# Performance work log

Hardware: AMD Instinct MI355X
Metric: run time of the kernel (lower is better)

## Reference

```python
import jax, jax.numpy as jnp
import numpy as np

B, H, W = 1, 64, 64  # N = B*H*W = 4096


def setup_inputs() -> dict:
    key = jax.random.key(0)
    pred_logits = jax.random.normal(key, (B, 1, H, W), dtype=jnp.float32)
    return {"pred_logits": pred_logits}


def _spectral_relaxation(feats):
    # feats: (N, 2) rows [max_conf, residual_dispersion]
    # L2-normalize rows (torch F.normalize: clamp norm at 1e-12)
    nrm = jnp.maximum(jnp.linalg.norm(feats, axis=1, keepdims=True), 1e-12)
    fn = feats / nrm
    A = fn @ fn.T                      # (N, N) rank<=2 gram affinity
    d = A.sum(axis=1)                  # degree vector
    dis = 1.0 / (jnp.sqrt(d) + 1e-10)  # D^{-1/2} diagonal
    # L_norm = D^{-1/2} (diag(d) - A) D^{-1/2}
    Ln = jnp.diag(d * dis * dis) - (dis[:, None] * A) * dis[None, :]
    w, V = jnp.linalg.eigh(Ln)
    fied = V[:, 1]                     # Fiedler vector (2nd smallest eigenvalue)
    # deterministic sign canonicalization (eigh sign is arbitrary)
    idx = jnp.argmax(jnp.abs(fied))
    fied = fied * jnp.where(fied[idx] >= 0, 1.0, -1.0)
    return (fied - fied.min()) / (fied.max() - fied.min() + 1e-10)


def reference(pred_logits):
    b, _, h, w = pred_logits.shape
    p = jax.nn.sigmoid(pred_logits)
    max_conf = jnp.maximum(p, 1.0 - p)               # (B,1,H,W)
    v = (1.0 - max_conf) / (max_conf + 1e-10)        # residual dispersion
    feats = jnp.concatenate([max_conf, v], axis=1)   # (B,2,H,W)
    feats_flat = feats.transpose(0, 2, 3, 1).reshape(-1, 2)  # (N,2)
    scores = _spectral_relaxation(feats_flat)        # (N,)
    reliability_mask = scores.reshape(b, h, w, 1).transpose(0, 3, 1, 2)
    return reliability_mask
```

## Files before the change

kernel.cpp:

```cpp
#include <hip/hip_runtime.h>
#include <math.h>


constexpr int N  = 4096;
constexpr int NT = 1024;
constexpr int PT = N / NT;
constexpr int NW = NT / 64;

__device__ __forceinline__ void block_reduce_sum(const double* vals, int m,
                                                 double* scr, double* outv) {
    const int lane = threadIdx.x & 63;
    const int wave = threadIdx.x >> 6;
    for (int j = 0; j < m; ++j) {
        double v = vals[j];
        #pragma unroll
        for (int off = 32; off > 0; off >>= 1) v += __shfl_down(v, off, 64);
        if (lane == 0) scr[j * NW + wave] = v;
    }
    __syncthreads();
    if (wave == 0) {
        for (int j = 0; j < m; ++j) {
            double v = (lane < NW) ? scr[j * NW + lane] : 0.0;
            #pragma unroll
            for (int off = 8; off > 0; off >>= 1) v += __shfl_down(v, off, 64);
            if (lane == 0) outv[j] = v;
        }
    }
    __syncthreads();
}

__global__ __launch_bounds__(NT) void spectral_kernel(const float* __restrict__ logits,
                                                      float* __restrict__ out) {
    __shared__ double s_scr[NW * 3];
    __shared__ double s_bc[4];
    __shared__ unsigned long long s_key[NW];
    __shared__ float s_mm[NW * 2];
    __shared__ float s_sign;

    const int tid  = threadIdx.x;
    const int lane = tid & 63;
    const int wave = tid >> 6;

    float c[PT], s[PT], dis[PT];

    double acc[3];
    acc[0] = 0.0; acc[1] = 0.0;
    #pragma unroll
    for (int k = 0; k < PT; ++k) {
        const int i = tid + k * NT;
        float x  = logits[i];
        float p  = 1.0f / (1.0f + expf(-x));
        float mc = fmaxf(p, 1.0f - p);
        float v  = (1.0f - mc) / (mc + 1e-10f);
        float nr = fmaxf(sqrtf(mc * mc + v * v), 1e-12f);
        c[k] = mc / nr;
        s[k] = v / nr;
        acc[0] += (double)c[k];
        acc[1] += (double)s[k];
    }
    block_reduce_sum(acc, 2, s_scr, s_bc);
    const double Sc = s_bc[0];
    const double Ss = s_bc[1];

    acc[0] = 0.0; acc[1] = 0.0; acc[2] = 0.0;
    #pragma unroll
    for (int k = 0; k < PT; ++k) {
        double d  = (double)c[k] * Sc + (double)s[k] * Ss;
        double di = 1.0 / (sqrt(d) + 1e-10);
        dis[k] = (float)di;
        double gc = di * (double)c[k];
        double gs = di * (double)s[k];
        acc[0] += gc * gc;
        acc[1] += gc * gs;
        acc[2] += gs * gs;
    }
    block_reduce_sum(acc, 3, s_scr, s_bc);
    const double C11 = s_bc[0], C12 = s_bc[1], C22 = s_bc[2];

    double tr   = C11 + C22;
    double df   = C11 - C22;
    double disc = sqrt(df * df + 4.0 * C12 * C12);
    double lmin = 0.5 * (tr - disc);
    double ux1 = C12,        uy1 = lmin - C11;
    double ux2 = lmin - C22, uy2 = C12;
    double n1 = ux1 * ux1 + uy1 * uy1;
    double n2 = ux2 * ux2 + uy2 * uy2;
    double ux, uy, nn;
    if (n1 >= n2) { ux = ux1; uy = uy1; nn = n1; }
    else          { ux = ux2; uy = uy2; nn = n2; }
    double inv = 1.0 / sqrt(nn > 1e-300 ? nn : 1e-300);
    ux *= inv; uy *= inv;
    double sfac = 1.0 / sqrt(lmin > 1e-300 ? lmin : 1e-300);

    float fl[PT];
    float vmin = 3.402823466e38f, vmax = -3.402823466e38f;
    unsigned long long key = 0ULL;
    #pragma unroll
    for (int k = 0; k < PT; ++k) {
        const unsigned i = (unsigned)(tid + k * NT);
        double fv = (double)dis[k] * ((double)c[k] * ux + (double)s[k] * uy) * sfac;
        float f = (float)fv;
        fl[k] = f;
        vmin = fminf(vmin, f);
        vmax = fmaxf(vmax, f);
        unsigned af = __float_as_uint(fabsf(f));
        unsigned long long kk =
            ((unsigned long long)af << 32) | (unsigned long long)(0xFFFFFFFFu - i);
        key = (kk > key) ? kk : key;
    }
    #pragma unroll
    for (int off = 32; off > 0; off >>= 1) {
        vmin = fminf(vmin, __shfl_down(vmin, off, 64));
        vmax = fmaxf(vmax, __shfl_down(vmax, off, 64));
        unsigned long long ok = __shfl_down(key, off, 64);
        key = (ok > key) ? ok : key;
    }
    if (lane == 0) { s_mm[wave] = vmin; s_mm[NW + wave] = vmax; s_key[wave] = key; }
    __syncthreads();
    if (wave == 0) {
        vmin = (lane < NW) ? s_mm[lane]      :  3.402823466e38f;
        vmax = (lane < NW) ? s_mm[NW + lane] : -3.402823466e38f;
        key  = (lane < NW) ? s_key[lane]     : 0ULL;
        #pragma unroll
        for (int off = 8; off > 0; off >>= 1) {
            vmin = fminf(vmin, __shfl_down(vmin, off, 64));
            vmax = fmaxf(vmax, __shfl_down(vmax, off, 64));
            unsigned long long ok = __shfl_down(key, off, 64);
            key = (ok > key) ? ok : key;
        }
        if (lane == 0) { s_mm[0] = vmin; s_mm[1] = vmax; s_key[0] = key; }
    }
    __syncthreads();
    vmin = s_mm[0]; vmax = s_mm[1]; key = s_key[0];
    const unsigned widx = 0xFFFFFFFFu - (unsigned)(key & 0xFFFFFFFFULL);

    #pragma unroll
    for (int k = 0; k < PT; ++k) {
        const unsigned i = (unsigned)(tid + k * NT);
        if (i == widx) s_sign = (fl[k] >= 0.0f) ? 1.0f : -1.0f;
    }
    __syncthreads();
    const float sgn  = s_sign;
    const float gmin = (sgn > 0.0f) ? vmin : -vmax;
    const float gmax = (sgn > 0.0f) ? vmax : -vmin;
    const float invr = 1.0f / (gmax - gmin + 1e-10f);

    #pragma unroll
    for (int k = 0; k < PT; ++k) {
        const int i = tid + k * NT;
        out[i] = (sgn * fl[k] - gmin) * invr;
    }
}

extern "C" void kernel_launch(void* const* d_in, const int* in_sizes, int n_in,
                              void* d_out, int out_size, void* d_ws, size_t ws_size,
                              hipStream_t stream) {
    const float* logits = (const float*)d_in[0];
    float* out = (float*)d_out;
    spectral_kernel<<<dim3(1), dim3(NT), 0, stream>>>(logits, out);
}
```

Before: 60.35 us.

## Use float reductions, float4 I/O, fast exp, and pack sign into argmax key

Replaces the double-precision per-element math and block reductions with float arithmetic, keeping only the tiny 2x2 eigen solve in double. Loads and stores switch to float4 so each thread handles four contiguous elements. expf becomes __expf. The sign of the largest-magnitude entry is packed into the argmax key, which removes a shared write and one barrier. Together these aim to cut FP64 throughput cost and synchronization in this single-block kernel, at the risk of small precision differences against the reference.

```diff
diff --git a/kernel.cpp b/kernel.cpp
--- a/kernel.cpp
+++ b/kernel.cpp
@@ -7,12 +7,12 @@
 constexpr int PT = N / NT;
 constexpr int NW = NT / 64;
 
-__device__ __forceinline__ void block_reduce_sum(const double* vals, int m,
-                                                 double* scr, double* outv) {
+__device__ __forceinline__ void block_reduce_sum_f(const float* vals, int m,
+                                                   float* scr, float* outv) {
     const int lane = threadIdx.x & 63;
     const int wave = threadIdx.x >> 6;
     for (int j = 0; j < m; ++j) {
-        double v = vals[j];
+        float v = vals[j];
         #pragma unroll
         for (int off = 32; off > 0; off >>= 1) v += __shfl_down(v, off, 64);
         if (lane == 0) scr[j * NW + wave] = v;
@@ -20,7 +20,7 @@
     __syncthreads();
     if (wave == 0) {
         for (int j = 0; j < m; ++j) {
-            double v = (lane < NW) ? scr[j * NW + lane] : 0.0;
+            float v = (lane < NW) ? scr[j * NW + lane] : 0.0f;
             #pragma unroll
             for (int off = 8; off > 0; off >>= 1) v += __shfl_down(v, off, 64);
             if (lane == 0) outv[j] = v;
@@ -29,13 +29,12 @@
     __syncthreads();
 }
 
-__global__ __launch_bounds__(NT) void spectral_kernel(const float* __restrict__ logits,
-                                                      float* __restrict__ out) {
-    __shared__ double s_scr[NW * 3];
-    __shared__ double s_bc[4];
+__global__ __launch_bounds__(NT) void spectral_kernel(const float4* __restrict__ logits4,
+                                                      float4* __restrict__ out4) {
+    __shared__ float s_scr[NW * 3];
+    __shared__ float s_bc[4];
     __shared__ unsigned long long s_key[NW];
     __shared__ float s_mm[NW * 2];
-    __shared__ float s_sign;
 
     const int tid  = threadIdx.x;
     const int lane = tid & 63;
@@ -43,40 +42,41 @@
 
     float c[PT], s[PT], dis[PT];
 
-    double acc[3];
-    acc[0] = 0.0; acc[1] = 0.0;
+    const float4 x4 = logits4[tid];
+    const float xs[PT] = {x4.x, x4.y, x4.z, x4.w};
+    float acc[3];
+    acc[0] = 0.0f; acc[1] = 0.0f;
     #pragma unroll
     for (int k = 0; k < PT; ++k) {
-        const int i = tid + k * NT;
-        float x  = logits[i];
-        float p  = 1.0f / (1.0f + expf(-x));
+        float x  = xs[k];
+        float p  = 1.0f / (1.0f + __expf(-x));
         float mc = fmaxf(p, 1.0f - p);
         float v  = (1.0f - mc) / (mc + 1e-10f);
         float nr = fmaxf(sqrtf(mc * mc + v * v), 1e-12f);
         c[k] = mc / nr;
         s[k] = v / nr;
-        acc[0] += (double)c[k];
-        acc[1] += (double)s[k];
+        acc[0] += c[k];
+        acc[1] += s[k];
     }
-    block_reduce_sum(acc, 2, s_scr, s_bc);
-    const double Sc = s_bc[0];
-    const double Ss = s_bc[1];
+    block_reduce_sum_f(acc, 2, s_scr, s_bc);
+    const float Sc = s_bc[0];
+    const float Ss = s_bc[1];
 
-    acc[0] = 0.0; acc[1] = 0.0; acc[2] = 0.0;
+    acc[0] = 0.0f; acc[1] = 0.0f; acc[2] = 0.0f;
     #pragma unroll
     for (int k = 0; k < PT; ++k) {
-        double d  = (double)c[k] * Sc + (double)s[k] * Ss;
-        double di = 1.0 / (sqrt(d) + 1e-10);
-        dis[k] = (float)di;
-        double gc = di * (double)c[k];
-        double gs = di * (double)s[k];
+        float d  = c[k] * Sc + s[k] * Ss;
+        float di = 1.0f / (sqrtf(d) + 1e-10f);
+        dis[k] = di;
+        float gc = di * c[k];
+        float gs = di * s[k];
         acc[0] += gc * gc;
         acc[1] += gc * gs;
         acc[2] += gs * gs;
     }
-    block_reduce_sum(acc, 3, s_scr, s_bc);
-    const double C11 = s_bc[0], C12 = s_bc[1], C22 = s_bc[2];
+    block_reduce_sum_f(acc, 3, s_scr, s_bc);
 
+    const double C11 = (double)s_bc[0], C12 = (double)s_bc[1], C22 = (double)s_bc[2];
     double tr   = C11 + C22;
     double df   = C11 - C22;
     double disc = sqrt(df * df + 4.0 * C12 * C12);
@@ -85,27 +85,28 @@
     double ux2 = lmin - C22, uy2 = C12;
     double n1 = ux1 * ux1 + uy1 * uy1;
     double n2 = ux2 * ux2 + uy2 * uy2;
-    double ux, uy, nn;
-    if (n1 >= n2) { ux = ux1; uy = uy1; nn = n1; }
-    else          { ux = ux2; uy = uy2; nn = n2; }
+    double uxd, uyd, nn;
+    if (n1 >= n2) { uxd = ux1; uyd = uy1; nn = n1; }
+    else          { uxd = ux2; uyd = uy2; nn = n2; }
     double inv = 1.0 / sqrt(nn > 1e-300 ? nn : 1e-300);
-    ux *= inv; uy *= inv;
-    double sfac = 1.0 / sqrt(lmin > 1e-300 ? lmin : 1e-300);
+    double sf  = inv / sqrt(lmin > 1e-300 ? lmin : 1e-300);
+    const float ux = (float)(uxd * sf);
+    const float uy = (float)(uyd * sf);
 
     float fl[PT];
     float vmin = 3.402823466e38f, vmax = -3.402823466e38f;
     unsigned long long key = 0ULL;
     #pragma unroll
     for (int k = 0; k < PT; ++k) {
-        const unsigned i = (unsigned)(tid + k * NT);
-        double fv = (double)dis[k] * ((double)c[k] * ux + (double)s[k] * uy) * sfac;
-        float f = (float)fv;
+        const unsigned i = (unsigned)(tid * PT + k);
+        float f = dis[k] * (c[k] * ux + s[k] * uy);
         fl[k] = f;
         vmin = fminf(vmin, f);
         vmax = fmaxf(vmax, f);
         unsigned af = __float_as_uint(fabsf(f));
-        unsigned long long kk =
-            ((unsigned long long)af << 32) | (unsigned long long)(0xFFFFFFFFu - i);
+        unsigned long long kk = ((unsigned long long)af << 33)
+                              | ((unsigned long long)(0xFFFFFFFFu - i) << 1)
+                              | (unsigned long long)(f >= 0.0f ? 1u : 0u);
         key = (kk > key) ? kk : key;
     }
     #pragma unroll
@@ -131,31 +132,24 @@
         if (lane == 0) { s_mm[0] = vmin; s_mm[1] = vmax; s_key[0] = key; }
     }
     __syncthreads();
-    vmin = s_mm[0]; vmax = s_mm[1]; key = s_key[0];
-    const unsigned widx = 0xFFFFFFFFu - (unsigned)(key & 0xFFFFFFFFULL);
-
-    #pragma unroll
-    for (int k = 0; k < PT; ++k) {
-        const unsigned i = (unsigned)(tid + k * NT);
-        if (i == widx) s_sign = (fl[k] >= 0.0f) ? 1.0f : -1.0f;
-    }
-    __syncthreads();
-    const float sgn  = s_sign;
+    vmin = s_mm[0]; vmax = s_mm[1];
+    const float sgn  = (s_key[0] & 1ULL) ? 1.0f : -1.0f;
     const float gmin = (sgn > 0.0f) ? vmin : -vmax;
     const float gmax = (sgn > 0.0f) ? vmax : -vmin;
     const float invr = 1.0f / (gmax - gmin + 1e-10f);
 
-    #pragma unroll
-    for (int k = 0; k < PT; ++k) {
-        const int i = tid + k * NT;
-        out[i] = (sgn * fl[k] - gmin) * invr;
-    }
+    float4 o;
+    o.x = (sgn * fl[0] - gmin) * invr;
+    o.y = (sgn * fl[1] - gmin) * invr;
+    o.z = (sgn * fl[2] - gmin) * invr;
+    o.w = (sgn * fl[3] - gmin) * invr;
+    out4[tid] = o;
 }
 
 extern "C" void kernel_launch(void* const* d_in, const int* in_sizes, int n_in,
                               void* d_out, int out_size, void* d_ws, size_t ws_size,
                               hipStream_t stream) {
-    const float* logits = (const float*)d_in[0];
-    float* out = (float*)d_out;
-    spectral_kernel<<<dim3(1), dim3(NT), 0, stream>>>(logits, out);
+    const float4* logits4 = (const float4*)d_in[0];
+    float4* out4 = (float4*)d_out;
+    spectral_kernel<<<dim3(1), dim3(NT), 0, stream>>>(logits4, out4);
 }
```

After: 59.25 us. No clear change (-1.8%).
